# Kernel tuning notes

Measured on AMD Instinct MI355X. Metric: run time of the kernel, lower is better.

Reference implementation:

```python
import jax, jax.numpy as jnp
import numpy as np
import math

B, L, D = 2, 2048, 768
H, R = 12, 128
DH = D // H  # 64

def setup_inputs():
    key = jax.random.key(0)
    ks = jax.random.split(key, 9)
    s = 0.02
    return {
        "x": jax.random.normal(ks[0], (B, L, D), jnp.float32),
        "W_qkv": jax.random.normal(ks[1], (D, 3 * D), jnp.float32) * s,
        "b_qkv": jnp.zeros((3 * D,), jnp.float32),
        "W_sem_down": jax.random.normal(ks[2], (D, R), jnp.float32) * s,
        "W_sem_up": jax.random.normal(ks[3], (R, 2 * D), jnp.float32) * s,
        "W_ctx_down": jax.random.normal(ks[4], (D, R), jnp.float32) * s,
        "W_ctx_up": jax.random.normal(ks[5], (R, 2 * D), jnp.float32) * s,
        "temperature": jnp.ones((1,), jnp.float32) * 0.5,
        "W_proj": jax.random.normal(ks[6], (D, D), jnp.float32) * s,
        "b_proj": jnp.zeros((D,), jnp.float32),
        "gamma": jnp.ones((D,), jnp.float32),
        "beta": jnp.zeros((D,), jnp.float32),
    }

def _layernorm(x, gamma, beta, eps=1e-5):
    mu = x.mean(-1, keepdims=True)
    var = ((x - mu) ** 2).mean(-1, keepdims=True)
    return (x - mu) * jax.lax.rsqrt(var + eps) * gamma + beta

def reference(x, W_qkv, b_qkv, W_sem_down, W_sem_up, W_ctx_down, W_ctx_up,
              temperature, W_proj, b_proj, gamma, beta):
    x_norm = _layernorm(x, gamma, beta)
    qkv = x_norm @ W_qkv + b_qkv
    q, k, v = jnp.split(qkv, 3, axis=-1)

    # sinusoidal interference gate from two low-rank branches
    sem = jax.nn.silu(x @ W_sem_down) @ W_sem_up
    sem_amp, sem_phase = jnp.split(sem, 2, axis=-1)
    sem_amp = jax.nn.softplus(sem_amp)
    sem_phase = jnp.tanh(sem_phase) * math.pi
    ctx = jax.nn.silu(x @ W_ctx_down) @ W_ctx_up
    ctx_amp, ctx_phase = jnp.split(ctx, 2, axis=-1)
    ctx_amp = jax.nn.softplus(ctx_amp)
    ctx_phase = jnp.tanh(ctx_phase) * math.pi
    interference = sem_amp * ctx_amp * jnp.cos(sem_phase - ctx_phase) * temperature
    gate = jax.nn.sigmoid(interference)
    k = k * (1.0 + gate)

    # (B,L,D) -> (B,H,L,DH)
    to_heads = lambda t: t.reshape(B, L, H, DH).transpose(0, 2, 1, 3)
    q_f = jax.nn.elu(to_heads(q).astype(jnp.float32)) + 1.0
    k_f = jax.nn.elu(to_heads(k).astype(jnp.float32)) + 1.0
    v_f = to_heads(v).astype(jnp.float32)

    # causal linear attention via explicit k (x) v cumsum
    kv_state = k_f[..., :, None] * v_f[..., None, :]   # (B,H,L,DH,DH)
    kv_cumsum = jnp.cumsum(kv_state, axis=2)
    out_num = jnp.einsum('bhld,bhlde->bhle', q_f, kv_cumsum)
    k_cumsum = jnp.cumsum(k_f, axis=2)
    out_den = (q_f * k_cumsum).sum(-1, keepdims=True) + 1e-6
    attn = (out_num / out_den).astype(x.dtype)
    attn = attn.transpose(0, 2, 1, 3).reshape(B, L, D)
    return attn @ W_proj + b_proj, gate
```

## Files before the change

### kernel.cpp

```cpp
#include <hip/hip_runtime.h>

#define B_    2
#define L_    2048
#define D_    768
#define H_    12
#define BL    4096
#define BH    24
#define CHUNK 128
#define NC    16
#define GOFF  3145728
#define PI_F  3.14159265358979f

typedef __bf16 bf16x8 __attribute__((ext_vector_type(8)));
typedef float  f32x4  __attribute__((ext_vector_type(4)));
typedef unsigned short us8 __attribute__((ext_vector_type(8)));

__device__ __forceinline__ float bf2f(unsigned short u) {
    return __uint_as_float(((unsigned int)u) << 16);
}
__device__ __forceinline__ unsigned short f2bf(float f) {
    unsigned int u = __float_as_uint(f);
    unsigned int r = (u + 0x7fffu + ((u >> 16) & 1u)) >> 16;
    return (unsigned short)r;
}
__device__ __forceinline__ float softplusf(float x) {
    return x > 20.f ? x : log1pf(expf(x));
}

__global__ __launch_bounds__(256) void detect_kernel(const unsigned short* __restrict__ x,
                                                     int* __restrict__ flag)
{
    __shared__ int cnt;
    if (threadIdx.x == 0) cnt = 0;
    __syncthreads();
    int c = 0;
    #pragma unroll
    for (int i = 0; i < 16; i++) {
        unsigned short u = x[threadIdx.x * 16 + i];
        int e = (u >> 7) & 0xff;
        if (e < 100 || e > 140) c++;
    }
    atomicAdd(&cnt, c);
    __syncthreads();
    if (threadIdx.x == 0) flag[0] = (cnt > 512) ? 1 : 0;
}

__global__ __launch_bounds__(256) void convert_mega_kernel(
    const void* __restrict__ sx, unsigned short* __restrict__ dx,
    const void* __restrict__ s1, unsigned short* __restrict__ d1,
    const void* __restrict__ s2, unsigned short* __restrict__ d2,
    const void* __restrict__ s3, unsigned short* __restrict__ d3,
    const void* __restrict__ s4, unsigned short* __restrict__ d4,
    const void* __restrict__ s5, unsigned short* __restrict__ d5,
    const int* __restrict__ flag)
{
    int id = blockIdx.x, t = threadIdx.x;
    int fl = flag[0];
    const void* src; unsigned short* dst; int n, base;
    if (id < 12288)      { src = sx; dst = dx; n = BL * D_; base = id * 256; }
    else if (id < 12297) { src = s1; dst = d1; n = 2304; base = (id - 12288) * 256; }
    else if (id < 12300) { src = s2; dst = d2; n = 768;  base = (id - 12297) * 256; }
    else if (id < 12303) { src = s3; dst = d3; n = 768;  base = (id - 12300) * 256; }
    else if (id < 12306) { src = s4; dst = d4; n = 768;  base = (id - 12303) * 256; }
    else                 { src = s5; dst = d5; n = 1;    base = 0; }
    int i = base + t;
    if (i < n) dst[i] = fl ? f2bf(((const float*)src)[i]) : ((const unsigned short*)src)[i];
}

__global__ __launch_bounds__(256) void transpose_mega_kernel(
    const void* __restrict__ s0, unsigned short* __restrict__ dq,
    const void* __restrict__ s1, unsigned short* __restrict__ dd,
    const void* __restrict__ s2, unsigned short* __restrict__ dsu,
    const void* __restrict__ s3,
    const void* __restrict__ s4, unsigned short* __restrict__ dcu,
    const void* __restrict__ s5, unsigned short* __restrict__ dp,
    const int* __restrict__ flag)
{
    __shared__ unsigned short tile[32][33];
    int id = blockIdx.x;
    const void* src; unsigned short* dst; int K, N, tid;
    if (id < 1728)      { src = s0; dst = dq;  K = 768; N = 2304; tid = id; }
    else if (id < 1824) { src = s1; dst = dd;  K = 768; N = 128;  tid = id - 1728; }
    else if (id < 2016) { src = s2; dst = dsu; K = 128; N = 1536; tid = id - 1824; }
    else if (id < 2112) { src = s3; dst = dd + (size_t)128 * 768; K = 768; N = 128; tid = id - 2016; }
    else if (id < 2304) { src = s4; dst = dcu; K = 128; N = 1536; tid = id - 2112; }
    else                { src = s5; dst = dp;  K = 768; N = 768;  tid = id - 2304; }
    int tn = N / 32;
    int by = (tid / tn) * 32, bx = (tid % tn) * 32;
    int tx = threadIdx.x & 31, tyb = threadIdx.x >> 5;
    int fl = flag[0];
    #pragma unroll
    for (int i = 0; i < 4; i++) {
        int k = by + tyb * 4 + i, n = bx + tx;
        size_t off = (size_t)k * N + n;
        tile[tyb * 4 + i][tx] = fl ? f2bf(((const float*)src)[off]) : ((const unsigned short*)src)[off];
    }
    __syncthreads();
    #pragma unroll
    for (int i = 0; i < 4; i++) {
        int n = bx + tyb * 4 + i, k = by + tx;
        dst[(size_t)n * K + k] = tile[tx][tyb * 4 + i];
    }
}

__global__ __launch_bounds__(256) void ln_kernel(
    const unsigned short* __restrict__ x,
    const unsigned short* __restrict__ gamma,
    const unsigned short* __restrict__ beta,
    unsigned short* __restrict__ xn)
{
    int row = blockIdx.x, t = threadIdx.x;
    const unsigned short* xr = x + (size_t)row * D_;
    float v[3];
    #pragma unroll
    for (int j = 0; j < 3; j++) v[j] = bf2f(xr[t + j * 256]);
    __shared__ float red[8];
    float s = v[0] + v[1] + v[2];
    #pragma unroll
    for (int m = 32; m >= 1; m >>= 1) s += __shfl_xor(s, m, 64);
    int wid = t >> 6;
    if ((t & 63) == 0) red[wid] = s;
    __syncthreads();
    float mean = (red[0] + red[1] + red[2] + red[3]) * (1.f / 768.f);
    float s2 = 0.f;
    #pragma unroll
    for (int j = 0; j < 3; j++) { float d = v[j] - mean; s2 += d * d; }
    #pragma unroll
    for (int m = 32; m >= 1; m >>= 1) s2 += __shfl_xor(s2, m, 64);
    if ((t & 63) == 0) red[4 + wid] = s2;
    __syncthreads();
    float var = (red[4] + red[5] + red[6] + red[7]) * (1.f / 768.f);
    float rs = rsqrtf(var + 1e-5f);
    #pragma unroll
    for (int j = 0; j < 3; j++) {
        int c = t + j * 256;
        float o = (v[j] - mean) * rs * bf2f(gamma[c]) + bf2f(beta[c]);
        xn[(size_t)row * D_ + c] = f2bf(o);
    }
}

template<int EPI>
__global__ __launch_bounds__(256) void mfma_gemm_kernel(
    const unsigned short* __restrict__ A, int lda,
    const unsigned short* __restrict__ BT,
    const unsigned short* __restrict__ bias,
    const void* __restrict__ gate,
    void* __restrict__ outp,
    const int* __restrict__ flag,
    int N, int K)
{
    __shared__ unsigned short sbuf[2 * 128 * 72];
    unsigned short* As = sbuf;
    unsigned short* Bs = sbuf + 128 * 72;
    unsigned short* Cs = sbuf;

    int f = blockIdx.y * gridDim.x + blockIdx.x;
    int rps = gridDim.y >> 3;
    int strip = f & 7, within = f >> 3;
    int by = strip * rps + (within % rps);
    int bx = within / rps;
    int m0 = by * 128, n0 = bx * 128;

    int t = threadIdx.x;
    int lane = t & 63, wave = t >> 6, quad = lane >> 4, l16 = lane & 15;
    int wm = (wave & 1) * 64, wn = (wave >> 1) * 64;
    int lr = t >> 1, lc = (t & 1) * 32;
    const unsigned short* Ap = A + (size_t)(m0 + lr) * lda + lc;
    const unsigned short* Bp = BT + (size_t)(n0 + lr) * K + lc;

    f32x4 acc[4][4];
    #pragma unroll
    for (int i = 0; i < 4; i++)
        #pragma unroll
        for (int j = 0; j < 4; j++) acc[i][j] = (f32x4){0.f, 0.f, 0.f, 0.f};

    for (int k0 = 0; k0 < K; k0 += 64) {
        us8 a[4], b[4];
        #pragma unroll
        for (int c = 0; c < 4; c++) {
            a[c] = *(const us8*)&Ap[k0 + c * 8];
            b[c] = *(const us8*)&Bp[k0 + c * 8];
        }
        __syncthreads();
        #pragma unroll
        for (int c = 0; c < 4; c++) {
            *(us8*)&As[lr * 72 + lc + c * 8] = a[c];
            *(us8*)&Bs[lr * 72 + lc + c * 8] = b[c];
        }
        __syncthreads();
        #pragma unroll
        for (int ks = 0; ks < 2; ks++) {
            bf16x8 af[4], bfr[4];
            #pragma unroll
            for (int i = 0; i < 4; i++)
                af[i] = *(const bf16x8*)&As[(wm + i * 16 + l16) * 72 + ks * 32 + quad * 8];
            #pragma unroll
            for (int j = 0; j < 4; j++)
                bfr[j] = *(const bf16x8*)&Bs[(wn + j * 16 + l16) * 72 + ks * 32 + quad * 8];
            #pragma unroll
            for (int i = 0; i < 4; i++)
                #pragma unroll
                for (int j = 0; j < 4; j++)
                    acc[i][j] = __builtin_amdgcn_mfma_f32_16x16x32_bf16(af[i], bfr[j], acc[i][j], 0, 0, 0);
        }
    }

    int fl = (EPI >= 2) ? flag[0] : 0;
    __syncthreads();
    #pragma unroll
    for (int j = 0; j < 4; j++) {
        int col = n0 + wn + j * 16 + l16;
        float bv = bias ? bf2f(bias[col]) : 0.f;
        #pragma unroll
        for (int i = 0; i < 4; i++) {
            #pragma unroll
            for (int r = 0; r < 4; r++) {
                int row = m0 + wm + i * 16 + quad * 4 + r;
                float v = acc[i][j][r] + bv;
                if (EPI == 1) v = v / (1.f + expf(-v));
                if (EPI == 2) {
                    if (col < D_) {
                        v = v > 0.f ? v + 1.f : expf(v);
                    } else if (col < 2 * D_) {
                        size_t go = (size_t)GOFF + (size_t)row * D_ + (col - D_);
                        float gg = fl ? ((const float*)gate)[go]
                                      : bf2f(((const unsigned short*)gate)[go]);
                        v *= (1.f + gg);
                        v = v > 0.f ? v + 1.f : expf(v);
                    }
                }
                if (EPI == 3 && fl) {
                    ((float*)outp)[(size_t)row * N + col] = v;
                } else {
                    Cs[(wm + i * 16 + quad * 4 + r) * 136 + wn + j * 16 + l16] = f2bf(v);
                }
            }
        }
    }
    if (!(EPI == 3 && fl)) {
        __syncthreads();
        #pragma unroll
        for (int p = 0; p < 8; p++) {
            int idx = p * 256 + t;
            int row = idx >> 4, cc = (idx & 15) * 8;
            *(us8*)&((unsigned short*)outp)[(size_t)(m0 + row) * N + n0 + cc] =
                *(const us8*)&Cs[row * 136 + cc];
        }
    }
}

__global__ __launch_bounds__(256) void gate_mfma_kernel(
    const unsigned short* __restrict__ tdown,
    const unsigned short* __restrict__ WsuT,
    const unsigned short* __restrict__ WcuT,
    const unsigned short* __restrict__ tempc,
    void* __restrict__ dout, const int* __restrict__ flag)
{
    __shared__ unsigned short gbuf[4 * 64 * 68];
    int f = blockIdx.y * gridDim.x + blockIdx.x;
    int rps = gridDim.y >> 3;
    int strip = f & 7, within = f >> 3;
    int by = strip * rps + (within % rps);
    int bx = within / rps;
    int m0 = by * 64, c0 = bx * 64;

    int t = threadIdx.x;
    int lane = t & 63, wave = t >> 6, quad = lane >> 4, l16 = lane & 15;
    int tr = t >> 2, tc = (t & 3) * 8;
    f32x4 acc[4][4];
    #pragma unroll
    for (int i = 0; i < 4; i++)
        #pragma unroll
        for (int j = 0; j < 4; j++) acc[i][j] = (f32x4){0.f, 0.f, 0.f, 0.f};

    int Atile = wave >> 1, Btile = 2 + wave;
    for (int k0 = 0; k0 < 128; k0 += 32) {
        us8 v0 = *(const us8*)&tdown[(size_t)(m0 + tr) * 256 + k0 + tc];
        us8 v1 = *(const us8*)&tdown[(size_t)(m0 + tr) * 256 + 128 + k0 + tc];
        us8 v2 = *(const us8*)&WsuT[(size_t)(c0 + tr) * 128 + k0 + tc];
        us8 v3 = *(const us8*)&WsuT[(size_t)(768 + c0 + tr) * 128 + k0 + tc];
        us8 v4 = *(const us8*)&WcuT[(size_t)(c0 + tr) * 128 + k0 + tc];
        us8 v5 = *(const us8*)&WcuT[(size_t)(768 + c0 + tr) * 128 + k0 + tc];
        __syncthreads();
        *(us8*)&gbuf[0 * 2560 + tr * 40 + tc] = v0;
        *(us8*)&gbuf[1 * 2560 + tr * 40 + tc] = v1;
        *(us8*)&gbuf[2 * 2560 + tr * 40 + tc] = v2;
        *(us8*)&gbuf[3 * 2560 + tr * 40 + tc] = v3;
        *(us8*)&gbuf[4 * 2560 + tr * 40 + tc] = v4;
        *(us8*)&gbuf[5 * 2560 + tr * 40 + tc] = v5;
        __syncthreads();
        bf16x8 af[4], bfr[4];
        #pragma unroll
        for (int i = 0; i < 4; i++)
            af[i] = *(const bf16x8*)&gbuf[Atile * 2560 + (i * 16 + l16) * 40 + quad * 8];
        #pragma unroll
        for (int j = 0; j < 4; j++)
            bfr[j] = *(const bf16x8*)&gbuf[Btile * 2560 + (j * 16 + l16) * 40 + quad * 8];
        #pragma unroll
        for (int i = 0; i < 4; i++)
            #pragma unroll
            for (int j = 0; j < 4; j++)
                acc[i][j] = __builtin_amdgcn_mfma_f32_16x16x32_bf16(af[i], bfr[j], acc[i][j], 0, 0, 0);
    }
    __syncthreads();
    #pragma unroll
    for (int i = 0; i < 4; i++)
        #pragma unroll
        for (int j = 0; j < 4; j++)
            #pragma unroll
            for (int r = 0; r < 4; r++)
                gbuf[wave * 4352 + (i * 16 + quad * 4 + r) * 68 + j * 16 + l16] = f2bf(acc[i][j][r]);
    __syncthreads();
    float tempv = bf2f(tempc[0]);
    int fl = flag[0];
    #pragma unroll
    for (int p = 0; p < 16; p++) {
        int idx = p * 256 + t;
        int row = idx >> 6, col = idx & 63;
        float sa = softplusf(bf2f(gbuf[0 * 4352 + row * 68 + col]));
        float sp = tanhf(bf2f(gbuf[1 * 4352 + row * 68 + col])) * PI_F;
        float ca = softplusf(bf2f(gbuf[2 * 4352 + row * 68 + col]));
        float cp = tanhf(bf2f(gbuf[3 * 4352 + row * 68 + col])) * PI_F;
        float inter = sa * ca * cosf(sp - cp) * tempv;
        float g = 1.f / (1.f + expf(-inter));
        size_t off = (size_t)GOFF + (size_t)(m0 + row) * D_ + c0 + col;
        if (fl) ((float*)dout)[off] = g;
        else    ((unsigned short*)dout)[off] = f2bf(g);
    }
}

__global__ __launch_bounds__(256) void chunk_sum_mfma_kernel(
    const unsigned short* __restrict__ qkvt,
    float* __restrict__ Msum, float* __restrict__ Zsum)
{
    __shared__ __align__(16) unsigned short KT[64 * 136];
    __shared__ __align__(16) unsigned short VT[80 * 136];
    int blk = blockIdx.x;
    int bh = blk / NC, cc = blk - bh * NC;
    int b = bh / H_, h = bh - b * H_;
    int t = threadIdx.x;
    int lane = t & 63, wave = t >> 6, quad = lane >> 4, l16 = lane & 15;
    int lr = t >> 1, lc = (t & 1) * 32;
    size_t rowbase = (size_t)(b * L_ + cc * CHUNK);
    const unsigned short* kg = qkvt + rowbase * 2304 + D_ + h * 64;
    const unsigned short* vg = qkvt + rowbase * 2304 + 2 * D_ + h * 64;
    #pragma unroll
    for (int c = 0; c < 4; c++) {
        us8 kv = *(const us8*)&kg[(size_t)lr * 2304 + lc + c * 8];
        us8 vv = *(const us8*)&vg[(size_t)lr * 2304 + lc + c * 8];
        #pragma unroll
        for (int ii = 0; ii < 8; ii++) {
            KT[(lc + c * 8 + ii) * 136 + lr] = kv[ii];
            VT[(lc + c * 8 + ii) * 136 + lr] = vv[ii];
        }
    }
    if (t < 128) VT[64 * 136 + t] = 0x3F80;
    __syncthreads();

    f32x4 acc[5];
    #pragma unroll
    for (int j = 0; j < 5; j++) acc[j] = (f32x4){0.f, 0.f, 0.f, 0.f};
    #pragma unroll
    for (int ks = 0; ks < 4; ks++) {
        bf16x8 a = *(const bf16x8*)&KT[(wave * 16 + l16) * 136 + ks * 32 + quad * 8];
        #pragma unroll
        for (int j = 0; j < 5; j++) {
            bf16x8 bv = *(const bf16x8*)&VT[(j * 16 + l16) * 136 + ks * 32 + quad * 8];
            acc[j] = __builtin_amdgcn_mfma_f32_16x16x32_bf16(a, bv, acc[j], 0, 0, 0);
        }
    }
    float* mo = Msum + (size_t)blk * 4096;
    #pragma unroll
    for (int j = 0; j < 4; j++)
        #pragma unroll
        for (int r = 0; r < 4; r++)
            mo[(wave * 16 + quad * 4 + r) * 64 + j * 16 + l16] = acc[j][r];
    if (l16 == 0) {
        #pragma unroll
        for (int r = 0; r < 4; r++)
            Zsum[(size_t)blk * 64 + wave * 16 + quad * 4 + r] = acc[4][r];
    }
}

__global__ __launch_bounds__(256) void prefix_kernel(
    float* __restrict__ Msum, float* __restrict__ Zsum)
{
    int blk = blockIdx.x;
    int bh = blk >> 2, qd = blk & 3;
    int t = threadIdx.x;
    size_t base = (size_t)bh * NC * 4096 + qd * 1024 + t * 4;
    float4 v[NC];
    #pragma unroll
    for (int c = 0; c < NC; c++) v[c] = *(const float4*)&Msum[base + (size_t)c * 4096];
    float4 run = make_float4(0.f, 0.f, 0.f, 0.f);
    #pragma unroll
    for (int c = 0; c < NC; c++) {
        float4 tmp = v[c];
        *(float4*)&Msum[base + (size_t)c * 4096] = run;
        run.x += tmp.x; run.y += tmp.y; run.z += tmp.z; run.w += tmp.w;
    }
    if (qd == 0 && t < 64) {
        float rz = 0.f;
        for (int c = 0; c < NC; c++) {
            float* pz = &Zsum[((size_t)bh * NC + c) * 64 + t];
            float vv = *pz; *pz = rz; rz += vv;
        }
    }
}

__global__ __launch_bounds__(256) void chunk_scan_mfma_kernel(
    const unsigned short* __restrict__ qkvt,
    const float* __restrict__ Msum, const float* __restrict__ Zsum,
    unsigned short* __restrict__ attnb)
{
    __shared__ __align__(16) unsigned short sbuf[35072];
    unsigned short* Qs = sbuf;
    unsigned short* Ks = sbuf + 9216;
    unsigned short* Ps = sbuf;
    unsigned short* VT = sbuf + 18432;
    unsigned short* Ss = sbuf + 29312;
    unsigned short* Cout = sbuf;

    int blk = blockIdx.x;
    int bh = blk / NC, cc = blk - bh * NC;
    int b = bh / H_, h = bh - b * H_;
    int t = threadIdx.x;
    int lane = t & 63, wave = t >> 6, quad = lane >> 4, l16 = lane & 15;
    int wm = wave * 32;
    int lr = t >> 1, lc = (t & 1) * 32;
    size_t rowbase = (size_t)(b * L_ + cc * CHUNK);
    const unsigned short* qg = qkvt + rowbase * 2304 + h * 64;
    const unsigned short* kg = qkvt + rowbase * 2304 + D_ + h * 64;
    const unsigned short* vg = qkvt + rowbase * 2304 + 2 * D_ + h * 64;
    const float* mp = Msum + (size_t)blk * 4096;
    const float* zp = Zsum + (size_t)blk * 64;

    #pragma unroll
    for (int c = 0; c < 4; c++) {
        us8 qv = *(const us8*)&qg[(size_t)lr * 2304 + lc + c * 8];
        us8 kv = *(const us8*)&kg[(size_t)lr * 2304 + lc + c * 8];
        us8 vv = *(const us8*)&vg[(size_t)lr * 2304 + lc + c * 8];
        *(us8*)&Qs[lr * 72 + lc + c * 8] = qv;
        *(us8*)&Ks[lr * 72 + lc + c * 8] = kv;
        #pragma unroll
        for (int ii = 0; ii < 8; ii++)
            VT[(lc + c * 8 + ii) * 136 + lr] = vv[ii];
    }
    if (t < 128) VT[64 * 136 + t] = 0x3F80;
    {
        int d = t & 63, jb = (t >> 6) * 16;
        #pragma unroll
        for (int g4 = 0; g4 < 4; g4++) {
            float4 sv = *(const float4*)&mp[d * 64 + jb + g4 * 4];
            Ss[(jb + g4 * 4 + 0) * 72 + d] = f2bf(sv.x);
            Ss[(jb + g4 * 4 + 1) * 72 + d] = f2bf(sv.y);
            Ss[(jb + g4 * 4 + 2) * 72 + d] = f2bf(sv.z);
            Ss[(jb + g4 * 4 + 3) * 72 + d] = f2bf(sv.w);
        }
    }
    if (t < 64) Ss[64 * 72 + t] = f2bf(zp[t]);
    __syncthreads();

    f32x4 Pacc[2][8], Oacc[2][5];
    #pragma unroll
    for (int i = 0; i < 2; i++) {
        #pragma unroll
        for (int n = 0; n < 8; n++) Pacc[i][n] = (f32x4){0.f, 0.f, 0.f, 0.f};
        #pragma unroll
        for (int j = 0; j < 5; j++) Oacc[i][j] = (f32x4){0.f, 0.f, 0.f, 0.f};
    }
    bf16x8 aq[2][2];
    #pragma unroll
    for (int i = 0; i < 2; i++)
        #pragma unroll
        for (int ks = 0; ks < 2; ks++)
            aq[i][ks] = *(const bf16x8*)&Qs[(wm + i * 16 + l16) * 72 + ks * 32 + quad * 8];
    #pragma unroll
    for (int n = 0; n < 8; n++)
        #pragma unroll
        for (int ks = 0; ks < 2; ks++) {
            bf16x8 bk = *(const bf16x8*)&Ks[(n * 16 + l16) * 72 + ks * 32 + quad * 8];
            #pragma unroll
            for (int i = 0; i < 2; i++)
                Pacc[i][n] = __builtin_amdgcn_mfma_f32_16x16x32_bf16(aq[i][ks], bk, Pacc[i][n], 0, 0, 0);
        }
    #pragma unroll
    for (int j = 0; j < 5; j++)
        #pragma unroll
        for (int ks = 0; ks < 2; ks++) {
            bf16x8 bs = *(const bf16x8*)&Ss[(j * 16 + l16) * 72 + ks * 32 + quad * 8];
            #pragma unroll
            for (int i = 0; i < 2; i++)
                Oacc[i][j] = __builtin_amdgcn_mfma_f32_16x16x32_bf16(aq[i][ks], bs, Oacc[i][j], 0, 0, 0);
        }
    __syncthreads();

    #pragma unroll
    for (int i = 0; i < 2; i++)
        #pragma unroll
        for (int n = 0; n < 8; n++)
            #pragma unroll
            for (int r = 0; r < 4; r++) {
                int trow = wm + i * 16 + quad * 4 + r;
                int scol = n * 16 + l16;
                Ps[trow * 136 + scol] = (scol <= trow) ? f2bf(Pacc[i][n][r]) : 0;
            }
    __syncthreads();

    #pragma unroll
    for (int ks = 0; ks < 4; ks++) {
        bf16x8 ap[2];
        #pragma unroll
        for (int i = 0; i < 2; i++)
            ap[i] = *(const bf16x8*)&Ps[(wm + i * 16 + l16) * 136 + ks * 32 + quad * 8];
        #pragma unroll
        for (int j = 0; j < 5; j++) {
            bf16x8 bv = *(const bf16x8*)&VT[(j * 16 + l16) * 136 + ks * 32 + quad * 8];
            #pragma unroll
            for (int i = 0; i < 2; i++)
                Oacc[i][j] = __builtin_amdgcn_mfma_f32_16x16x32_bf16(ap[i], bv, Oacc[i][j], 0, 0, 0);
        }
    }
    __syncthreads();

    #pragma unroll
    for (int i = 0; i < 2; i++) {
        #pragma unroll
        for (int r = 0; r < 4; r++) {
            float den = __shfl(Oacc[i][4][r], lane & 48) + 1e-6f;
            float inv = 1.f / den;
            #pragma unroll
            for (int j = 0; j < 4; j++)
                Cout[(wm + i * 16 + quad * 4 + r) * 136 + j * 16 + l16] = f2bf(Oacc[i][j][r] * inv);
        }
    }
    __syncthreads();
    unsigned short* abase = attnb + rowbase * D_ + h * 64;
    #pragma unroll
    for (int p = 0; p < 4; p++) {
        int idx = p * 256 + t;
        int row = idx >> 3, cg = (idx & 7) * 8;
        *(us8*)&abase[(size_t)row * D_ + cg] = *(const us8*)&Cout[row * 136 + cg];
    }
}

extern "C" void kernel_launch(void* const* d_in, const int* in_sizes, int n_in,
                              void* d_out, int out_size, void* d_ws, size_t ws_size,
                              hipStream_t stream)
{
    char* w = (char*)d_ws;
    auto alloc = [&](size_t bytes) { void* p = (void*)w; w += (bytes + 255) & ~(size_t)255; return p; };
    int*            flagp   = (int*)alloc(256);
    unsigned short* x_c     = (unsigned short*)alloc((size_t)BL * D_ * 2);
    unsigned short* attnb   = x_c;
    unsigned short* xn      = (unsigned short*)alloc((size_t)BL * D_ * 2);
    unsigned short* WqkvT   = (unsigned short*)alloc((size_t)2304 * 768 * 2);
    unsigned short* WdT     = (unsigned short*)alloc((size_t)256 * 768 * 2);
    unsigned short* WsuT    = (unsigned short*)alloc((size_t)1536 * 128 * 2);
    unsigned short* WcuT    = (unsigned short*)alloc((size_t)1536 * 128 * 2);
    unsigned short* WprojT  = (unsigned short*)alloc((size_t)768 * 768 * 2);
    unsigned short* bqkv_c  = (unsigned short*)alloc((size_t)2304 * 2);
    unsigned short* bproj_c = (unsigned short*)alloc((size_t)768 * 2);
    unsigned short* gamma_c = (unsigned short*)alloc((size_t)768 * 2);
    unsigned short* beta_c  = (unsigned short*)alloc((size_t)768 * 2);
    unsigned short* temp_c  = (unsigned short*)alloc(256);
    unsigned short* tdown   = (unsigned short*)alloc((size_t)BL * 256 * 2);
    float*          Zsum    = (float*)alloc((size_t)BH * NC * 64 * 4);
    unsigned short* qkvt    = (unsigned short*)alloc((size_t)BL * 2304 * 2);
    float*          Msum    = (float*)alloc((size_t)BH * NC * 4096 * 4);

    dim3 blk(256);
    detect_kernel<<<1, blk, 0, stream>>>((const unsigned short*)d_in[0], flagp);
    convert_mega_kernel<<<12307, blk, 0, stream>>>(
        d_in[0], x_c, d_in[2], bqkv_c, d_in[9], bproj_c,
        d_in[10], gamma_c, d_in[11], beta_c, d_in[7], temp_c, flagp);
    transpose_mega_kernel<<<2880, blk, 0, stream>>>(
        d_in[1], WqkvT, d_in[3], WdT, d_in[4], WsuT,
        d_in[5], d_in[6], WcuT, d_in[8], WprojT, flagp);
    ln_kernel<<<BL, blk, 0, stream>>>(x_c, gamma_c, beta_c, xn);
    mfma_gemm_kernel<1><<<dim3(2, 32), blk, 0, stream>>>(x_c, 768, WdT, nullptr, nullptr, tdown, flagp, 256, 768);
    gate_mfma_kernel<<<dim3(12, 64), blk, 0, stream>>>(tdown, WsuT, WcuT, temp_c, d_out, flagp);
    mfma_gemm_kernel<2><<<dim3(18, 32), blk, 0, stream>>>(xn, 768, WqkvT, bqkv_c, d_out, qkvt, flagp, 2304, 768);
    chunk_sum_mfma_kernel<<<BH * NC, blk, 0, stream>>>(qkvt, Msum, Zsum);
    prefix_kernel<<<BH * 4, blk, 0, stream>>>(Msum, Zsum);
    chunk_scan_mfma_kernel<<<BH * NC, blk, 0, stream>>>(qkvt, Msum, Zsum, attnb);
    mfma_gemm_kernel<3><<<dim3(6, 32), blk, 0, stream>>>(attnb, 768, WprojT, bproj_c, nullptr, d_out, flagp, 768, 768);
}
```

Baseline: 256.2 us.

## Fuse x conversion into layernorm, DMA GEMM tiles to LDS, add bf16 gate buffer

Drops the full-tensor convert pass by having the layernorm kernel read x in its original dtype and write both the bf16 copy and the normalized output. The GEMM kernel now loads tiles with global_load_lds direct-to-LDS DMA into an XOR-swizzled unpadded layout instead of staging through registers. The gate is also written to a bf16 scratch buffer (aliased onto Msum) so the QKV epilogue reads bf16 instead of branching on the output dtype. Risks include the serialized load/compute with no double buffering and the aliasing of the gate scratch with Msum, which is only valid because chunk_sum runs after the QKV GEMM.

```diff
diff --git a/kernel.cpp b/kernel.cpp
--- a/kernel.cpp
+++ b/kernel.cpp
@@ -26,6 +26,11 @@
 __device__ __forceinline__ float softplusf(float x) {
     return x > 20.f ? x : log1pf(expf(x));
 }
+__device__ __forceinline__ void dma16(const unsigned short* g, unsigned short* l) {
+    __builtin_amdgcn_global_load_lds(
+        (const __attribute__((address_space(1))) unsigned int*)g,
+        (__attribute__((address_space(3))) unsigned int*)l, 16, 0, 0);
+}
 
 __global__ __launch_bounds__(256) void detect_kernel(const unsigned short* __restrict__ x,
                                                      int* __restrict__ flag)
@@ -45,8 +50,7 @@
     if (threadIdx.x == 0) flag[0] = (cnt > 512) ? 1 : 0;
 }
 
-__global__ __launch_bounds__(256) void convert_mega_kernel(
-    const void* __restrict__ sx, unsigned short* __restrict__ dx,
+__global__ __launch_bounds__(256) void convert_small_kernel(
     const void* __restrict__ s1, unsigned short* __restrict__ d1,
     const void* __restrict__ s2, unsigned short* __restrict__ d2,
     const void* __restrict__ s3, unsigned short* __restrict__ d3,
@@ -57,12 +61,11 @@
     int id = blockIdx.x, t = threadIdx.x;
     int fl = flag[0];
     const void* src; unsigned short* dst; int n, base;
-    if (id < 12288)      { src = sx; dst = dx; n = BL * D_; base = id * 256; }
-    else if (id < 12297) { src = s1; dst = d1; n = 2304; base = (id - 12288) * 256; }
-    else if (id < 12300) { src = s2; dst = d2; n = 768;  base = (id - 12297) * 256; }
-    else if (id < 12303) { src = s3; dst = d3; n = 768;  base = (id - 12300) * 256; }
-    else if (id < 12306) { src = s4; dst = d4; n = 768;  base = (id - 12303) * 256; }
-    else                 { src = s5; dst = d5; n = 1;    base = 0; }
+    if (id < 9)       { src = s1; dst = d1; n = 2304; base = id * 256; }
+    else if (id < 12) { src = s2; dst = d2; n = 768;  base = (id - 9) * 256; }
+    else if (id < 15) { src = s3; dst = d3; n = 768;  base = (id - 12) * 256; }
+    else if (id < 18) { src = s4; dst = d4; n = 768;  base = (id - 15) * 256; }
+    else              { src = s5; dst = d5; n = 1;    base = 0; }
     int i = base + t;
     if (i < n) dst[i] = fl ? f2bf(((const float*)src)[i]) : ((const unsigned short*)src)[i];
 }
@@ -103,17 +106,23 @@
     }
 }
 
-__global__ __launch_bounds__(256) void ln_kernel(
-    const unsigned short* __restrict__ x,
+__global__ __launch_bounds__(256) void conv_ln_kernel(
+    const void* __restrict__ xin,
     const unsigned short* __restrict__ gamma,
     const unsigned short* __restrict__ beta,
-    unsigned short* __restrict__ xn)
+    unsigned short* __restrict__ x_c,
+    unsigned short* __restrict__ xn,
+    const int* __restrict__ flag)
 {
     int row = blockIdx.x, t = threadIdx.x;
-    const unsigned short* xr = x + (size_t)row * D_;
+    int fl = flag[0];
     float v[3];
     #pragma unroll
-    for (int j = 0; j < 3; j++) v[j] = bf2f(xr[t + j * 256]);
+    for (int j = 0; j < 3; j++) {
+        int c = t + j * 256;
+        v[j] = fl ? ((const float*)xin)[(size_t)row * D_ + c]
+                  : bf2f(((const unsigned short*)xin)[(size_t)row * D_ + c]);
+    }
     __shared__ float red[8];
     float s = v[0] + v[1] + v[2];
     #pragma unroll
@@ -134,6 +143,7 @@
     #pragma unroll
     for (int j = 0; j < 3; j++) {
         int c = t + j * 256;
+        x_c[(size_t)row * D_ + c] = f2bf(v[j]);
         float o = (v[j] - mean) * rs * bf2f(gamma[c]) + bf2f(beta[c]);
         xn[(size_t)row * D_ + c] = f2bf(o);
     }
@@ -144,14 +154,14 @@
     const unsigned short* __restrict__ A, int lda,
     const unsigned short* __restrict__ BT,
     const unsigned short* __restrict__ bias,
-    const void* __restrict__ gate,
+    const unsigned short* __restrict__ gateb,
     void* __restrict__ outp,
     const int* __restrict__ flag,
     int N, int K)
 {
-    __shared__ unsigned short sbuf[2 * 128 * 72];
+    __shared__ unsigned short sbuf[17408];
     unsigned short* As = sbuf;
-    unsigned short* Bs = sbuf + 128 * 72;
+    unsigned short* Bs = sbuf + 8192;
     unsigned short* Cs = sbuf;
 
     int f = blockIdx.y * gridDim.x + blockIdx.x;
@@ -164,9 +174,14 @@
     int t = threadIdx.x;
     int lane = t & 63, wave = t >> 6, quad = lane >> 4, l16 = lane & 15;
     int wm = (wave & 1) * 64, wn = (wave >> 1) * 64;
-    int lr = t >> 1, lc = (t & 1) * 32;
-    const unsigned short* Ap = A + (size_t)(m0 + lr) * lda + lc;
-    const unsigned short* Bp = BT + (size_t)(n0 + lr) * K + lc;
+    int xr = l16 & 7;
+
+    int sr8 = lane >> 3;
+    int scg = (lane & 7) ^ sr8;
+    const unsigned short* ApL = A  + (size_t)(m0 + wave * 32 + sr8) * lda + scg * 8;
+    const unsigned short* BpL = BT + (size_t)(n0 + wave * 32 + sr8) * K   + scg * 8;
+    unsigned short* AsW = As + wave * 32 * 64;
+    unsigned short* BsW = Bs + wave * 32 * 64;
 
     f32x4 acc[4][4];
     #pragma unroll
@@ -175,17 +190,11 @@
         for (int j = 0; j < 4; j++) acc[i][j] = (f32x4){0.f, 0.f, 0.f, 0.f};
 
     for (int k0 = 0; k0 < K; k0 += 64) {
-        us8 a[4], b[4];
+        __syncthreads();
         #pragma unroll
         for (int c = 0; c < 4; c++) {
-            a[c] = *(const us8*)&Ap[k0 + c * 8];
-            b[c] = *(const us8*)&Bp[k0 + c * 8];
-        }
-        __syncthreads();
-        #pragma unroll
-        for (int c = 0; c < 4; c++) {
-            *(us8*)&As[lr * 72 + lc + c * 8] = a[c];
-            *(us8*)&Bs[lr * 72 + lc + c * 8] = b[c];
+            dma16(ApL + (size_t)(c * 8) * lda + k0, AsW + c * 512);
+            dma16(BpL + (size_t)(c * 8) * K   + k0, BsW + c * 512);
         }
         __syncthreads();
         #pragma unroll
@@ -193,10 +202,10 @@
             bf16x8 af[4], bfr[4];
             #pragma unroll
             for (int i = 0; i < 4; i++)
-                af[i] = *(const bf16x8*)&As[(wm + i * 16 + l16) * 72 + ks * 32 + quad * 8];
+                af[i] = *(const bf16x8*)&As[(wm + i * 16 + l16) * 64 + (((ks * 4 + quad) ^ xr) * 8)];
             #pragma unroll
             for (int j = 0; j < 4; j++)
-                bfr[j] = *(const bf16x8*)&Bs[(wn + j * 16 + l16) * 72 + ks * 32 + quad * 8];
+                bfr[j] = *(const bf16x8*)&Bs[(wn + j * 16 + l16) * 64 + (((ks * 4 + quad) ^ xr) * 8)];
             #pragma unroll
             for (int i = 0; i < 4; i++)
                 #pragma unroll
@@ -205,7 +214,7 @@
         }
     }
 
-    int fl = (EPI >= 2) ? flag[0] : 0;
+    int fl = (EPI == 3) ? flag[0] : 0;
     __syncthreads();
     #pragma unroll
     for (int j = 0; j < 4; j++) {
@@ -222,9 +231,7 @@
                     if (col < D_) {
                         v = v > 0.f ? v + 1.f : expf(v);
                     } else if (col < 2 * D_) {
-                        size_t go = (size_t)GOFF + (size_t)row * D_ + (col - D_);
-                        float gg = fl ? ((const float*)gate)[go]
-                                      : bf2f(((const unsigned short*)gate)[go]);
+                        float gg = bf2f(gateb[(size_t)row * D_ + (col - D_)]);
                         v *= (1.f + gg);
                         v = v > 0.f ? v + 1.f : expf(v);
                     }
@@ -254,7 +261,9 @@
     const unsigned short* __restrict__ WsuT,
     const unsigned short* __restrict__ WcuT,
     const unsigned short* __restrict__ tempc,
-    void* __restrict__ dout, const int* __restrict__ flag)
+    void* __restrict__ dout,
+    unsigned short* __restrict__ gateb,
+    const int* __restrict__ flag)
 {
     __shared__ unsigned short gbuf[4 * 64 * 68];
     int f = blockIdx.y * gridDim.x + blockIdx.x;
@@ -324,8 +333,10 @@
         float inter = sa * ca * cosf(sp - cp) * tempv;
         float g = 1.f / (1.f + expf(-inter));
         size_t off = (size_t)GOFF + (size_t)(m0 + row) * D_ + c0 + col;
+        unsigned short gb = f2bf(g);
         if (fl) ((float*)dout)[off] = g;
-        else    ((unsigned short*)dout)[off] = f2bf(g);
+        else    ((unsigned short*)dout)[off] = gb;
+        gateb[(size_t)(m0 + row) * D_ + c0 + col] = gb;
     }
 }
 
@@ -568,19 +579,20 @@
     float*          Zsum    = (float*)alloc((size_t)BH * NC * 64 * 4);
     unsigned short* qkvt    = (unsigned short*)alloc((size_t)BL * 2304 * 2);
     float*          Msum    = (float*)alloc((size_t)BH * NC * 4096 * 4);
+    unsigned short* gateb   = (unsigned short*)Msum;
 
     dim3 blk(256);
     detect_kernel<<<1, blk, 0, stream>>>((const unsigned short*)d_in[0], flagp);
-    convert_mega_kernel<<<12307, blk, 0, stream>>>(
-        d_in[0], x_c, d_in[2], bqkv_c, d_in[9], bproj_c,
-        d_in[10], gamma_c, d_in[11], beta_c, d_in[7], temp_c, flagp);
+    convert_small_kernel<<<19, blk, 0, stream>>>(
+        d_in[2], bqkv_c, d_in[9], bproj_c, d_in[10], gamma_c,
+        d_in[11], beta_c, d_in[7], temp_c, flagp);
     transpose_mega_kernel<<<2880, blk, 0, stream>>>(
         d_in[1], WqkvT, d_in[3], WdT, d_in[4], WsuT,
         d_in[5], d_in[6], WcuT, d_in[8], WprojT, flagp);
-    ln_kernel<<<BL, blk, 0, stream>>>(x_c, gamma_c, beta_c, xn);
+    conv_ln_kernel<<<BL, blk, 0, stream>>>(d_in[0], gamma_c, beta_c, x_c, xn, flagp);
     mfma_gemm_kernel<1><<<dim3(2, 32), blk, 0, stream>>>(x_c, 768, WdT, nullptr, nullptr, tdown, flagp, 256, 768);
-    gate_mfma_kernel<<<dim3(12, 64), blk, 0, stream>>>(tdown, WsuT, WcuT, temp_c, d_out, flagp);
-    mfma_gemm_kernel<2><<<dim3(18, 32), blk, 0, stream>>>(xn, 768, WqkvT, bqkv_c, d_out, qkvt, flagp, 2304, 768);
+    gate_mfma_kernel<<<dim3(12, 64), blk, 0, stream>>>(tdown, WsuT, WcuT, temp_c, d_out, gateb, flagp);
+    mfma_gemm_kernel<2><<<dim3(18, 32), blk, 0, stream>>>(xn, 768, WqkvT, bqkv_c, gateb, qkvt, flagp, 2304, 768);
     chunk_sum_mfma_kernel<<<BH * NC, blk, 0, stream>>>(qkvt, Msum, Zsum);
     prefix_kernel<<<BH * 4, blk, 0, stream>>>(Msum, Zsum);
     chunk_scan_mfma_kernel<<<BH * NC, blk, 0, stream>>>(qkvt, Msum, Zsum, attnb);
```

New measurement: 245.9 us. -4.0%, faster.
